# Kernel optimization log

Hardware: AMD Instinct MI355X
Metric: run time of the kernel (lower is better)

The kernel has to match this reference:

```python
import jax, jax.numpy as jnp
import numpy as np

B, ORG, L = 128, 4, 2048
C1, C2 = 128, 64
K0, K1, K2 = 7, 5, 3
VQD, VQN = 64, 1024
CARD, NG = 32, 8
EPS = 1e-5


def _conv(x, w, groups=1):
    # 1D conv, stride 1, 'same' padding (k-1)//2, NCH layout, weight (O, I/g, K)
    p = (w.shape[-1] - 1) // 2
    return jax.lax.conv_general_dilated(
        x, w, (1,), [(p, p)],
        dimension_numbers=('NCH', 'OIH', 'NCH'), feature_group_count=groups)


def _tconv(x, w):
    # ConvTranspose1d(stride=1, padding=(k-1)//2) == conv with channel-transposed, spatially flipped kernel
    return _conv(x, jnp.flip(jnp.transpose(w, (1, 0, 2)), -1))


def _gn(x, g, b, groups=NG):
    Bx, C, T = x.shape
    xr = x.reshape(Bx, groups, C // groups, T)
    mu = xr.mean((2, 3), keepdims=True)
    var = xr.var((2, 3), keepdims=True)
    xn = ((xr - mu) * jax.lax.rsqrt(var + EPS)).reshape(Bx, C, T)
    return xn * g[None, :, None] + b[None, :, None]


def setup_inputs() -> dict:
    key = jax.random.key(0)
    ks = iter(jax.random.split(key, 32))
    w = lambda *s: jax.random.normal(next(ks), s, jnp.float32) * 0.05
    ones = lambda n: jnp.ones((n,), jnp.float32)
    zeros = lambda n: jnp.zeros((n,), jnp.float32)
    D = C1 // 2  # ResNeXt bottleneck width
    return dict(
        x=jax.random.normal(next(ks), (B, ORG, L), jnp.float32),
        w0=w(C1, ORG, K0), g0_g=ones(C1), g0_b=zeros(C1),
        wxa=w(D, C1, 1), gxa_g=ones(D), gxa_b=zeros(D),
        wxb=w(D, D // CARD, K1), gxb_g=ones(D), gxb_b=zeros(D),
        wxc=w(C1, D, 1), gxc_g=ones(C1), gxc_b=zeros(C1),
        w2=w(C2, C1, K2), bn2_g=ones(C2), bn2_b=zeros(C2),
        embed_w=jax.random.uniform(next(ks), (VQN, VQD), jnp.float32, -1.0 / VQD, 1.0 / VQD),
        wd2=w(C2, C1, K2), gd2_g=ones(C1), gd2_b=zeros(C1),
        wd1a=w(C1, C1, K1), gd1a_g=ones(C1), gd1a_b=zeros(C1),
        wd1b=w(C1, C1, K1), gd1b_g=ones(C1), gd1b_b=zeros(C1),
        wd0=w(C1, ORG, K0), bd0=zeros(ORG),
    )


def reference(x, w0, g0_g, g0_b, wxa, gxa_g, gxa_b, wxb, gxb_g, gxb_b,
              wxc, gxc_g, gxc_b, w2, bn2_g, bn2_b, embed_w,
              wd2, gd2_g, gd2_b, wd1a, gd1a_g, gd1a_b, wd1b, gd1b_g, gd1b_b,
              wd0, bd0):
    selu = jax.nn.selu

    # ---- encoder ----
    h = selu(_gn(_conv(x, w0), g0_g, g0_b))  # res0

    def resx(h):  # ResNeXt bottleneck, shared weights (module reuses self.resx)
        y = selu(_gn(_conv(h, wxa), gxa_g, gxa_b))
        y = selu(_gn(_conv(y, wxb, groups=CARD), gxb_g, gxb_b))
        y = _gn(_conv(y, wxc), gxc_g, gxc_b)
        return selu(h + y)

    pool = lambda t: t.reshape(t.shape[0], t.shape[1], -1, 2).max(-1)  # MaxPool1d(2)
    h = pool(resx(h))
    h = pool(resx(h))
    # res2: conv + BatchNorm (eval mode, running stats 0/1 -> affine)
    h = _conv(h, w2) * bn2_g[None, :, None] + bn2_b[None, :, None]

    # ---- vector quantization (vqc=True: quantize channel vectors) ----
    Bh, C, T = h.shape  # C == VQD
    Z = jnp.transpose(h, (0, 2, 1)).reshape(-1, VQD)  # [N, vq_dim]
    d = (jnp.sum(Z * Z, 1, keepdims=True) - 2.0 * (Z @ embed_w.T)
         + jnp.sum(embed_w * embed_w, 1)[None, :])  # [N, vq_num] squared L2
    j = jnp.argmin(d, axis=1)
    W_j = embed_w[j]
    commit_loss = jnp.mean(jnp.sum((Z - jax.lax.stop_gradient(W_j)) ** 2, -1))
    vq_loss = jnp.mean(jnp.sum((jax.lax.stop_gradient(Z) - W_j) ** 2, -1))
    hq = jnp.transpose(W_j.reshape(Bh, T, C), (0, 2, 1))  # back to [B, C, T]

    # ---- decoder ----
    up = lambda t: jnp.repeat(t, 2, axis=-1)  # nearest Upsample(x2)

    def deres1(h):  # basic residual block, shared weights (module reuses self.deres1)
        y = selu(_gn(_tconv(h, wd1a), gd1a_g, gd1a_b))
        y = _gn(_tconv(y, wd1b), gd1b_g, gd1b_b)
        return selu(h + y)

    h = selu(_gn(_tconv(hq, wd2), gd2_g, gd2_b))  # deres2
    h = deres1(up(h))
    h = deres1(up(h))
    recon = _tconv(h, wd0) + bd0[None, :, None]  # deres0 (with bias)
    return recon, commit_loss, vq_loss
```

## Files before the change

kernel.cpp:

```cpp
#include <hip/hip_runtime.h>
#include <math.h>

static constexpr int B_   = 128;
static constexpr int ORG_ = 4;
static constexpr int L_   = 2048;
static constexpr int C1_  = 128;
static constexpr int C2_  = 64;
static constexpr int NG_  = 8;
static constexpr int VQD_ = 64;
static constexpr int VQN_ = 1024;

typedef __attribute__((ext_vector_type(8))) short bf16x8;
typedef __attribute__((ext_vector_type(4))) float f32x4;

__device__ __forceinline__ float selu_f(float x) {
    const float scale = 1.0507009873554805f;
    const float alpha = 1.6732632423543772f;
    return scale * (x > 0.f ? x : alpha * expm1f(x));
}
__device__ __forceinline__ unsigned short f2bf(float x) {
    unsigned u = __float_as_uint(x);
    u = (u + 0x7FFFu + ((u >> 16) & 1u)) >> 16;
    return (unsigned short)u;
}

__global__ void wprep_kernel(const float* __restrict__ w, float* __restrict__ wT,
                             int CO, int cig, int K, int so, int si, int sk, int koff)
{
    int idx = blockIdx.x * 256 + threadIdx.x;
    int total = cig * K * CO;
    if (idx >= total) return;
    int o = idx % CO;
    int r = idx / CO;
    int i = r / K, k = r % K;
    wT[idx] = w[(long)o * so + (long)i * si + (long)k * sk + koff];
}

__global__ void wprep_mfma_kernel(const float* __restrict__ w, unsigned short* __restrict__ wb)
{
    int idx = blockIdx.x * 256 + threadIdx.x;
    if (idx >= 5 * 16 * 128 * 8) return;
    int j  = idx & 7;
    int o  = (idx >> 3) & 127;
    int kk = idx >> 10;
    int ig = kk & 3, ic = (kk >> 2) & 3, k = kk >> 4;
    int i  = ic * 32 + ig * 8 + j;
    wb[idx] = f2bf(w[(long)i * (128 * 5) + o * 5 + (4 - k)]);
}

__global__ void fill_kernel(float* p, float v, int n)
{
    int i = blockIdx.x * 256 + threadIdx.x;
    if (i < n) p[i] = v;
}

template<int K, int CO, int NTHR, int TT, int OT>
__global__ __launch_bounds__(NTHR) void conv_tile_kernel(
    const float* __restrict__ in, const float* __restrict__ wT,
    const float* __restrict__ scale, const float* __restrict__ bias,
    float* __restrict__ out,
    int CI, int T, int cig, int cog,
    const float* __restrict__ ist, const float* __restrict__ ig,
    const float* __restrict__ ibt, int icpg, int iselu,
    const float* __restrict__ res)
{
    constexpr int P    = (K - 1) / 2;
    constexpr int SPAN = TT + K - 1;
    constexpr int RS   = (SPAN + 3) & ~3;
    constexpr int NO   = CO / OT;
    constexpr int NT   = (CO * TT) / (NTHR * OT);
    constexpr int XW   = NT + K - 1;
    extern __shared__ float lds[];

    const int tile = blockIdx.x;
    const int b    = blockIdx.y;
    const int t0g  = tile * TT;
    const float* inb = in + (long)b * CI * T;

    for (int idx = threadIdx.x; idx < CI * SPAN; idx += NTHR) {
        int c = idx / SPAN, j = idx % SPAN;
        int tt = t0g + j - P;
        float v = 0.f;
        if (tt >= 0 && tt < T) {
            v = inb[(long)c * T + tt];
            if (ist) {
                const float* s = &ist[2 * (b * NG_ + c / icpg)];
                v = (v - s[0]) * s[1] * ig[c] + ibt[c];
                if (res) v += res[((long)b * CI + c) * T + tt];
                if (iselu) v = selu_f(v);
            }
        }
        lds[c * RS + j] = v;
    }
    __syncthreads();

    const int o0   = (threadIdx.x % NO) * OT;
    const int slot = threadIdx.x / NO;
    const int t0   = slot * NT;
    const int g    = o0 / cog;
    const float* wrow = wT + o0;

    float acc[OT][NT];
#pragma unroll
    for (int oo = 0; oo < OT; ++oo)
#pragma unroll
        for (int u = 0; u < NT; ++u) acc[oo][u] = 0.f;

    for (int i = 0; i < cig; ++i) {
        const int irow = g * cig + i;
        float xin[(XW + 3) & ~3];
        if constexpr (NT % 4 == 0) {
            constexpr int X4 = (XW + 3) / 4;
            const float4* l4 = reinterpret_cast<const float4*>(&lds[irow * RS + t0]);
#pragma unroll
            for (int j = 0; j < X4; ++j) {
                float4 v = l4[j];
                xin[4 * j]     = v.x;
                xin[4 * j + 1] = v.y;
                xin[4 * j + 2] = v.z;
                xin[4 * j + 3] = v.w;
            }
        } else {
#pragma unroll
            for (int j = 0; j < XW; ++j) xin[j] = lds[irow * RS + t0 + j];
        }
        float wk[OT][K];
#pragma unroll
        for (int oo = 0; oo < OT; ++oo)
#pragma unroll
            for (int k = 0; k < K; ++k) wk[oo][k] = wrow[(i * K + k) * CO + oo];
#pragma unroll
        for (int oo = 0; oo < OT; ++oo)
#pragma unroll
            for (int u = 0; u < NT; ++u)
#pragma unroll
                for (int k = 0; k < K; ++k)
                    acc[oo][u] = fmaf(xin[u + k], wk[oo][k], acc[oo][u]);
    }

#pragma unroll
    for (int oo = 0; oo < OT; ++oo) {
        const int o = o0 + oo;
        const float sc = scale ? scale[o] : 1.f;
        const float bi = bias  ? bias[o]  : 0.f;
        float* ob = out + ((long)b * CO + o) * T + t0g + t0;
#pragma unroll
        for (int u = 0; u < NT; ++u) ob[u] = acc[oo][u] * sc + bi;
    }
}

__global__ __launch_bounds__(256) void conv_mfma5_kernel(
    const float* __restrict__ in, const unsigned short* __restrict__ wb,
    float* __restrict__ out, int T,
    const float* __restrict__ ist, const float* __restrict__ ig_,
    const float* __restrict__ ibt, int icpg)
{
    constexpr int SPAN = 68, RSI = 136;
    __shared__ unsigned short xlds[SPAN * RSI];

    const int t0g = blockIdx.x * 64;
    const int b   = blockIdx.y;
    const float* inb = in + (long)b * 128 * T;

    for (int idx = threadIdx.x; idx < 128 * SPAN; idx += 256) {
        int i = idx / SPAN, j = idx % SPAN;
        int tt = t0g + j - 2;
        float v = 0.f;
        if (tt >= 0 && tt < T) {
            v = inb[(long)i * T + tt];
            if (ist) {
                const float* s = &ist[2 * (b * NG_ + i / icpg)];
                v = selu_f((v - s[0]) * s[1] * ig_[i] + ibt[i]);
            }
        }
        xlds[j * RSI + i] = f2bf(v);
    }
    __syncthreads();

    const int lane = threadIdx.x & 63;
    const int wid  = threadIdx.x >> 6;
    const int tw   = wid * 16;
    const int mr   = lane & 15;
    const int kg   = lane >> 4;

    f32x4 acc[8];
#pragma unroll
    for (int ot = 0; ot < 8; ++ot) acc[ot] = (f32x4){0.f, 0.f, 0.f, 0.f};

#pragma unroll
    for (int k = 0; k < 5; ++k) {
#pragma unroll
        for (int ic = 0; ic < 4; ++ic) {
            bf16x8 a = *(const bf16x8*)&xlds[(tw + mr + k) * RSI + ic * 32 + kg * 8];
            const unsigned short* wp = wb + (((k * 16 + ic * 4 + kg) * 128) + mr) * 8;
#pragma unroll
            for (int ot = 0; ot < 8; ++ot) {
                bf16x8 bfr = *(const bf16x8*)(wp + ot * 16 * 8);
                acc[ot] = __builtin_amdgcn_mfma_f32_16x16x32_bf16(a, bfr, acc[ot], 0, 0, 0);
            }
        }
    }

#pragma unroll
    for (int ot = 0; ot < 8; ++ot) {
        int o = ot * 16 + mr;
        float4 v = make_float4(acc[ot][0], acc[ot][1], acc[ot][2], acc[ot][3]);
        *(float4*)&out[((long)b * 128 + o) * T + t0g + tw + kg * 4] = v;
    }
}

__global__ __launch_bounds__(256) void gn_stats_kernel(
    const float* __restrict__ x, float* __restrict__ stats,
    int C, int T, int G)
{
    const int bg = blockIdx.x;
    const int cpg = C / G;
    const int b = bg / G, g = bg % G;
    const float* base = x + ((long)b * C + (long)g * cpg) * T;
    const long n4 = (long)cpg * T / 4;
    const float4* b4 = (const float4*)base;
    float s = 0.f, ss = 0.f;
    for (long i = threadIdx.x; i < n4; i += blockDim.x) {
        float4 v = b4[i];
        s += v.x + v.y + v.z + v.w;
        ss += v.x * v.x + v.y * v.y + v.z * v.z + v.w * v.w;
    }
#pragma unroll
    for (int off = 32; off; off >>= 1) {
        s  += __shfl_down(s, off);
        ss += __shfl_down(ss, off);
    }
    __shared__ float sh_s[4], sh_ss[4];
    const int wid = threadIdx.x >> 6, lane = threadIdx.x & 63;
    if (lane == 0) { sh_s[wid] = s; sh_ss[wid] = ss; }
    __syncthreads();
    if (threadIdx.x == 0) {
        float S = 0.f, SS = 0.f;
        for (int i = 0; i < 4; ++i) { S += sh_s[i]; SS += sh_ss[i]; }
        float inv_n = 1.f / (float)((long)cpg * T);
        float mu  = S * inv_n;
        float var = SS * inv_n - mu * mu;
        stats[2 * bg]     = mu;
        stats[2 * bg + 1] = rsqrtf(var + 1e-5f);
    }
}

__global__ __launch_bounds__(256) void pool_fused_kernel(
    const float* __restrict__ x, const float* __restrict__ xst,
    const float* __restrict__ xg, const float* __restrict__ xb, int xcpg,
    const float* __restrict__ r, const float* __restrict__ rst,
    const float* __restrict__ rg, const float* __restrict__ rb, int rcpg, int rselu,
    float* __restrict__ out, int C, int Tout, long total)
{
    for (long idx = blockIdx.x * (long)blockDim.x + threadIdx.x; idx < total;
         idx += (long)gridDim.x * blockDim.x) {
        const int to = (int)(idx % Tout);
        const int c  = (int)((idx / Tout) % C);
        const int b  = (int)(idx / ((long)Tout * C));
        const long base = ((long)b * C + c) * (2 * Tout);
        const float* sx = &xst[2 * (b * NG_ + c / xcpg)];
        const float xgc = sx[1] * xg[c], xbc = xb[c] - sx[0] * sx[1] * xg[c];
        float rgc = 1.f, rbc = 0.f;
        if (rst) {
            const float* sr = &rst[2 * (b * NG_ + c / rcpg)];
            rgc = sr[1] * rg[c]; rbc = rb[c] - sr[0] * sr[1] * rg[c];
        }
        float f[2];
#pragma unroll
        for (int q = 0; q < 2; ++q) {
            long t = base + 2 * to + q;
            float rv = r[t] * rgc + rbc;
            if (rst && rselu) rv = selu_f(rv);
            f[q] = selu_f(x[t] * xgc + xbc + rv);
        }
        out[((long)b * C + c) * Tout + to] = fmaxf(f[0], f[1]);
    }
}

__global__ __launch_bounds__(256) void up_fused_kernel(
    const float* __restrict__ x, const float* __restrict__ xst,
    const float* __restrict__ xg, const float* __restrict__ xb, int xcpg,
    const float* __restrict__ res,
    float* __restrict__ out, int C, int Tin, long total)
{
    for (long idx = blockIdx.x * (long)blockDim.x + threadIdx.x; idx < total;
         idx += (long)gridDim.x * blockDim.x) {
        const int t = (int)(idx % Tin);
        const int c = (int)((idx / Tin) % C);
        const int b = (int)(idx / ((long)Tin * C));
        const float* s = &xst[2 * (b * NG_ + c / xcpg)];
        float v = (x[idx] - s[0]) * s[1] * xg[c] + xb[c];
        if (res) v += res[idx];
        v = selu_f(v);
        float2* o2 = (float2*)(out + (((long)b * C + c) * Tin + t) * 2);
        *o2 = make_float2(v, v);
    }
}

__global__ void wnorm_kernel(const float* __restrict__ codes, float* __restrict__ wn)
{
    int j = blockIdx.x * 256 + threadIdx.x;
    if (j >= VQN_) return;
    const float* c = codes + (long)j * VQD_;
    float s = 0.f;
#pragma unroll
    for (int i = 0; i < VQD_; ++i) s = fmaf(c[i], c[i], s);
    wn[j] = s;
}

__global__ __launch_bounds__(256) void vq_argmin_kernel(
    const float* __restrict__ s0, const float* __restrict__ s1,
    float* __restrict__ bests, int* __restrict__ bjs,
    int T, int base, int init)
{
    __shared__ float tile[64 * 65];
    const int n0 = blockIdx.x * 64;
    const int b  = n0 / T;
    const int tb = n0 % T;
    const int p  = threadIdx.x;

    float best = 3.4e38f;
    int bj = base;
    if (p < 64 && !init) { best = bests[n0 + p]; bj = bjs[n0 + p]; }

    for (int half = 0; half < 2; ++half) {
        const float* S = half ? s1 : s0;
        for (int c0 = 0; c0 < 256; c0 += 64) {
            __syncthreads();
#pragma unroll
            for (int it = 0; it < 4; ++it) {
                int r  = it * 16 + (threadIdx.x >> 4);
                int c4 = threadIdx.x & 15;
                float4 v = *(const float4*)&S[((long)b * 256 + c0 + r) * T + tb + c4 * 4];
                tile[r * 65 + c4 * 4 + 0] = v.x;
                tile[r * 65 + c4 * 4 + 1] = v.y;
                tile[r * 65 + c4 * 4 + 2] = v.z;
                tile[r * 65 + c4 * 4 + 3] = v.w;
            }
            __syncthreads();
            if (p < 64) {
                int jb = base + half * 256 + c0;
#pragma unroll
                for (int c = 0; c < 64; ++c) {
                    float sv = tile[c * 65 + p];
                    if (sv < best) { best = sv; bj = jb + c; }
                }
            }
        }
    }
    if (p < 64) { bests[n0 + p] = best; bjs[n0 + p] = bj; }
}

__global__ __launch_bounds__(256) void vq_gather_kernel(
    const float* __restrict__ h, const float* __restrict__ codes,
    const int* __restrict__ bjs, float* __restrict__ hq, float* __restrict__ loss,
    int T)
{
    const int n0 = blockIdx.x * 64;
    const int b  = n0 / T;
    const int tb = n0 % T;
    __shared__ int sbj[64];
    if (threadIdx.x < 64) sbj[threadIdx.x] = bjs[n0 + threadIdx.x];
    __syncthreads();

    float l = 0.f;
#pragma unroll
    for (int r = 0; r < (VQD_ * 64) / 256; ++r) {
        int idx = r * 256 + (int)threadIdx.x;
        int c  = idx >> 6, tl = idx & 63;
        float wv = codes[(long)sbj[tl] * VQD_ + c];
        long off = ((long)b * VQD_ + c) * T + tb + tl;
        hq[off] = wv;
        float df = h[off] - wv;
        l = fmaf(df, df, l);
    }
#pragma unroll
    for (int off = 32; off; off >>= 1) l += __shfl_down(l, off);
    if ((threadIdx.x & 63) == 0) atomicAdd(loss, l);
}

__global__ void zero_kernel(float* p) { p[0] = 0.f; }

__global__ void finalize_kernel(const float* __restrict__ loss, float* __restrict__ out,
                                float invNP, long off)
{
    float v = loss[0] * invNP;
    out[off]     = v;
    out[off + 1] = v;
}

static inline int nblk(long total, int thr = 256, long cap = 262144) {
    long b = (total + thr - 1) / thr;
    if (b > cap) b = cap;
    if (b < 1) b = 1;
    return (int)b;
}
static inline int ldsz(int CI, int K, int TT = 64) {
    int span = TT + K - 1;
    int rs = (span + 3) & ~3;
    return CI * rs * 4;
}

struct WT {
    long w0, wxa, wxb, wxc, w2, wd2, wd0, total;
};
static WT wt_offsets() {
    WT o; long p = 0;
    o.w0   = p; p += (long)ORG_ * 7 * C1_;
    o.wxa  = p; p += (long)C1_ * 1 * (C1_ / 2);
    o.wxb  = p; p += 2L * 5 * (C1_ / 2);
    o.wxc  = p; p += (long)(C1_ / 2) * 1 * C1_;
    o.w2   = p; p += (long)C1_ * 3 * C2_;
    o.wd2  = p; p += (long)C2_ * 3 * C1_;
    o.wd0  = p; p += (long)C1_ * 7 * ORG_;
    o.total = p;
    return o;
}

static void run_chunk(const float* x, const float* const* W, const float* wt,
                      const WT& wo, const unsigned short* wbA, const unsigned short* wbB,
                      const float* wn, const float* wts, const float* neg2,
                      float* bests, int* bjs, float* out,
                      float* A, float* Bb, float* Cc, float* st, float* lossbuf,
                      int Bc, long nbuf, hipStream_t stream)
{
    const float* g0_g  = W[1];
    const float* g0_b  = W[2];
    const float* gxa_g = W[4];
    const float* gxa_b = W[5];
    const float* gxb_g = W[7];
    const float* gxb_b = W[8];
    const float* gxc_g = W[10];
    const float* gxc_b = W[11];
    const float* bn2_g = W[13];
    const float* bn2_b = W[14];
    const float* embed = W[15];
    const float* gd2_g = W[17];
    const float* gd2_b = W[18];
    const float* gd1a_g= W[20];
    const float* gd1a_b= W[21];
    const float* gd1b_g= W[23];
    const float* gd1b_b= W[24];
    const float* bd0   = W[26];

    const int D_ = C1_ / 2;
    const int SLOT = 2048;
    float* st0 = st + 0 * SLOT;
    float* st1 = st + 1 * SLOT;
    float* st2 = st + 2 * SLOT;
    float* st3 = st + 3 * SLOT;
    float* st4 = st + 4 * SLOT;
    float* st5 = st + 5 * SLOT;
    float* st6 = st + 6 * SLOT;

    const int nbg = Bc * NG_;

    int T = L_;

    conv_tile_kernel<7, 128, 512, 64, 1><<<dim3(T / 64, Bc), 512, ldsz(ORG_, 7), stream>>>(
        x, wt + wo.w0, nullptr, nullptr, A, ORG_, T, ORG_, C1_,
        nullptr, nullptr, nullptr, 0, 0, nullptr);
    gn_stats_kernel<<<nbg, 256, 0, stream>>>(A, st0, C1_, T, NG_);

    conv_tile_kernel<1, 64, 512, 64, 2><<<dim3(T / 64, Bc), 512, ldsz(C1_, 1), stream>>>(
        A, wt + wo.wxa, nullptr, nullptr, Bb, C1_, T, C1_, D_,
        st0, g0_g, g0_b, C1_ / NG_, 1, nullptr);
    gn_stats_kernel<<<nbg, 256, 0, stream>>>(Bb, st1, D_, T, NG_);

    conv_tile_kernel<5, 64, 512, 64, 1><<<dim3(T / 64, Bc), 512, ldsz(D_, 5), stream>>>(
        Bb, wt + wo.wxb, nullptr, nullptr, Bb + nbuf / 2, D_, T, 2, 2,
        st1, gxa_g, gxa_b, D_ / NG_, 1, nullptr);
    gn_stats_kernel<<<nbg, 256, 0, stream>>>(Bb + nbuf / 2, st2, D_, T, NG_);

    conv_tile_kernel<1, 128, 512, 64, 2><<<dim3(T / 64, Bc), 512, ldsz(D_, 1), stream>>>(
        Bb + nbuf / 2, wt + wo.wxc, nullptr, nullptr, Cc, D_, T, D_, C1_,
        st2, gxb_g, gxb_b, D_ / NG_, 1, nullptr);
    gn_stats_kernel<<<nbg, 256, 0, stream>>>(Cc, st3, C1_, T, NG_);

    {
        int Tout = T / 2;
        long tt = (long)Bc * C1_ * Tout;
        pool_fused_kernel<<<nblk(tt), 256, 0, stream>>>(
            Cc, st3, gxc_g, gxc_b, C1_ / NG_,
            A, st0, g0_g, g0_b, C1_ / NG_, 1,
            Bb, C1_, Tout, tt);
        T = Tout;
    }

    conv_tile_kernel<1, 64, 512, 64, 2><<<dim3(T / 64, Bc), 512, ldsz(C1_, 1), stream>>>(
        Bb, wt + wo.wxa, nullptr, nullptr, Cc, C1_, T, C1_, D_,
        nullptr, nullptr, nullptr, 0, 0, nullptr);
    gn_stats_kernel<<<nbg, 256, 0, stream>>>(Cc, st1, D_, T, NG_);

    conv_tile_kernel<5, 64, 512, 64, 1><<<dim3(T / 64, Bc), 512, ldsz(D_, 5), stream>>>(
        Cc, wt + wo.wxb, nullptr, nullptr, Cc + nbuf / 2, D_, T, 2, 2,
        st1, gxa_g, gxa_b, D_ / NG_, 1, nullptr);
    gn_stats_kernel<<<nbg, 256, 0, stream>>>(Cc + nbuf / 2, st2, D_, T, NG_);

    conv_tile_kernel<1, 128, 512, 64, 2><<<dim3(T / 64, Bc), 512, ldsz(D_, 1), stream>>>(
        Cc + nbuf / 2, wt + wo.wxc, nullptr, nullptr, A, D_, T, D_, C1_,
        st2, gxb_g, gxb_b, D_ / NG_, 1, nullptr);
    gn_stats_kernel<<<nbg, 256, 0, stream>>>(A, st3, C1_, T, NG_);

    {
        int Tout = T / 2;
        long tt = (long)Bc * C1_ * Tout;
        pool_fused_kernel<<<nblk(tt), 256, 0, stream>>>(
            A, st3, gxc_g, gxc_b, C1_ / NG_,
            Bb, nullptr, nullptr, nullptr, 0, 0,
            Cc, C1_, Tout, tt);
        T = Tout;
    }

    conv_tile_kernel<3, 64, 512, 64, 1><<<dim3(T / 64, Bc), 512, ldsz(C1_, 3), stream>>>(
        Cc, wt + wo.w2, bn2_g, bn2_b, Bb, C1_, T, C1_, C2_,
        nullptr, nullptr, nullptr, 0, 0, nullptr);

    {
        int NP = Bc * T;
        long half = nbuf / 2;
        for (int pass = 0; pass < 2; ++pass) {
            for (int q = 0; q < 2; ++q) {
                int base = pass * 512 + q * 256;
                conv_tile_kernel<1, 256, 512, 64, 4><<<dim3(T / 64, Bc), 512,
                                                       ldsz(VQD_, 1), stream>>>(
                    Bb, wts + (long)base * VQD_, neg2, wn + base, Cc + q * half,
                    VQD_, T, VQD_, 256,
                    nullptr, nullptr, nullptr, 0, 0, nullptr);
            }
            vq_argmin_kernel<<<NP / 64, 256, 0, stream>>>(
                Cc, Cc + half, bests, bjs, T, pass * 512, pass == 0 ? 1 : 0);
        }
        vq_gather_kernel<<<NP / 64, 256, 0, stream>>>(Bb, embed, bjs, A, lossbuf, T);
    }

    conv_tile_kernel<3, 128, 512, 64, 1><<<dim3(T / 64, Bc), 512, ldsz(C2_, 3), stream>>>(
        A, wt + wo.wd2, nullptr, nullptr, Bb, C2_, T, C2_, C1_,
        nullptr, nullptr, nullptr, 0, 0, nullptr);
    gn_stats_kernel<<<nbg, 256, 0, stream>>>(Bb, st4, C1_, T, NG_);

    {
        long tt = (long)Bc * C1_ * T;
        up_fused_kernel<<<nblk(tt), 256, 0, stream>>>(
            Bb, st4, gd2_g, gd2_b, C1_ / NG_, nullptr, Cc, C1_, T, tt);
        T *= 2;
    }

    conv_mfma5_kernel<<<dim3(T / 64, Bc), 256, 0, stream>>>(
        Cc, wbA, A, T, nullptr, nullptr, nullptr, 0);
    gn_stats_kernel<<<nbg, 256, 0, stream>>>(A, st5, C1_, T, NG_);

    conv_mfma5_kernel<<<dim3(T / 64, Bc), 256, 0, stream>>>(
        A, wbB, Bb, T, st5, gd1a_g, gd1a_b, C1_ / NG_);
    gn_stats_kernel<<<nbg, 256, 0, stream>>>(Bb, st6, C1_, T, NG_);

    {
        long tt = (long)Bc * C1_ * T;
        up_fused_kernel<<<nblk(tt), 256, 0, stream>>>(
            Bb, st6, gd1b_g, gd1b_b, C1_ / NG_, Cc, A, C1_, T, tt);
        T *= 2;
    }

    conv_mfma5_kernel<<<dim3(T / 64, Bc), 256, 0, stream>>>(
        A, wbA, Cc, T, nullptr, nullptr, nullptr, 0);
    gn_stats_kernel<<<nbg, 256, 0, stream>>>(Cc, st5, C1_, T, NG_);

    conv_mfma5_kernel<<<dim3(T / 64, Bc), 256, 0, stream>>>(
        Cc, wbB, Bb, T, st5, gd1a_g, gd1a_b, C1_ / NG_);
    gn_stats_kernel<<<nbg, 256, 0, stream>>>(Bb, st6, C1_, T, NG_);

    conv_tile_kernel<7, 4, 256, 64, 1><<<dim3(T / 64, Bc), 256, ldsz(C1_, 7), stream>>>(
        Bb, wt + wo.wd0, nullptr, bd0, out, C1_, T, C1_, ORG_,
        st6, gd1b_g, gd1b_b, C1_ / NG_, 1, A);
}

extern "C" void kernel_launch(void* const* d_in, const int* in_sizes, int n_in,
                              void* d_out, int out_size, void* d_ws, size_t ws_size,
                              hipStream_t stream) {
    const float* x = (const float*)d_in[0];
    const float* W[27];
    for (int i = 0; i < 27; ++i) W[i] = (const float*)d_in[i + 1];

    float* out = (float*)d_out;
    const WT wo = wt_offsets();

    const long WT_F32  = 262144;
    const long WB_F32  = 2 * 81920 / 2;
    const long WTS_F32 = VQN_ * VQD_;
    const long ST_F32  = 8 * 2048;
    const long PTS_MAX = (long)B_ * (L_ / 4);
    const long FIXED = WT_F32 + WB_F32 + 1024 + WTS_F32 + 256 + ST_F32 + 64
                     + PTS_MAX + PTS_MAX;
    int Bc = 0;
    for (int cand = B_; cand >= 1; cand >>= 1) {
        size_t need = ((size_t)FIXED + (size_t)3 * cand * C1_ * L_) * sizeof(float);
        if (need <= ws_size) { Bc = cand; break; }
    }
    if (Bc == 0) return;

    float* wt            = (float*)d_ws;
    unsigned short* wbA  = (unsigned short*)(wt + WT_F32);
    unsigned short* wbB  = wbA + 81920;
    float* wn            = wt + WT_F32 + WB_F32;
    float* wts           = wn + 1024;
    float* neg2          = wts + WTS_F32;
    float* st            = neg2 + 256;
    float* lossbuf       = st + ST_F32;
    float* bests         = lossbuf + 64;
    int*   bjs           = (int*)(bests + PTS_MAX);
    const long nbuf = (long)Bc * C1_ * L_;
    float* A  = (float*)(bjs + PTS_MAX);
    float* Bb = A + nbuf;
    float* Cc = Bb + nbuf;

    const int D_ = C1_ / 2;

    auto prep = [&](const float* w, long off, int CO, int cig, int K,
                    int so, int si, int sk, int koff) {
        int total = cig * K * CO;
        wprep_kernel<<<(total + 255) / 256, 256, 0, stream>>>(
            w, wt + off, CO, cig, K, so, si, sk, koff);
    };
    prep(W[0],  wo.w0,   C1_, ORG_, 7, ORG_ * 7, 7,        1,  0);
    prep(W[3],  wo.wxa,  D_,  C1_,  1, C1_,      1,        1,  0);
    prep(W[6],  wo.wxb,  D_,  2,    5, 2 * 5,    5,        1,  0);
    prep(W[9],  wo.wxc,  C1_, D_,   1, D_,       1,        1,  0);
    prep(W[12], wo.w2,   C2_, C1_,  3, C1_ * 3,  3,        1,  0);
    prep(W[16], wo.wd2,  C1_, C2_,  3, 3,        C1_ * 3, -1,  2);
    prep(W[25], wo.wd0,  ORG_, C1_, 7, 7,        ORG_ * 7, -1, 6);
    wprep_mfma_kernel<<<81920 / 256, 256, 0, stream>>>(W[19], wbA);
    wprep_mfma_kernel<<<81920 / 256, 256, 0, stream>>>(W[22], wbB);
    wnorm_kernel<<<(VQN_ + 255) / 256, 256, 0, stream>>>(W[15], wn);
    for (int q = 0; q < 4; ++q) {
        wprep_kernel<<<(256 * VQD_ + 255) / 256, 256, 0, stream>>>(
            W[15] + (long)q * 256 * VQD_, wts + (long)q * 256 * VQD_,
            256, VQD_, 1, VQD_, 1, 1, 0);
    }
    fill_kernel<<<1, 256, 0, stream>>>(neg2, -2.f, 256);

    zero_kernel<<<1, 1, 0, stream>>>(lossbuf);

    for (int b0 = 0; b0 < B_; b0 += Bc) {
        const float* xc = x + (long)b0 * ORG_ * L_;
        float* outc = out + (long)b0 * ORG_ * L_;
        run_chunk(xc, W, wt, wo, wbA, wbB, wn, wts, neg2, bests, bjs,
                  outc, A, Bb, Cc, st, lossbuf, Bc, nbuf, stream);
    }

    {
        float invNP = 1.f / (float)(B_ * (L_ / 4));
        finalize_kernel<<<1, 1, 0, stream>>>(lossbuf, out, invNP, (long)out_size - 2);
    }
}
```

Measured before the change: 2.384 ms.

## Fuse VQ distance argmin into conv epilogue and stage final conv weights in LDS

```diff
diff --git a/kernel.cpp b/kernel.cpp
--- a/kernel.cpp
+++ b/kernel.cpp
@@ -9,6 +9,7 @@
 static constexpr int NG_  = 8;
 static constexpr int VQD_ = 64;
 static constexpr int VQN_ = 1024;
+static constexpr long PTS_ = (long)B_ * (L_ / 4);
 
 typedef __attribute__((ext_vector_type(8))) short bf16x8;
 typedef __attribute__((ext_vector_type(4))) float f32x4;
@@ -54,7 +55,7 @@
     if (i < n) p[i] = v;
 }
 
-template<int K, int CO, int NTHR, int TT, int OT>
+template<int K, int CO, int NTHR, int TT, int OT, int VQ, int WL>
 __global__ __launch_bounds__(NTHR) void conv_tile_kernel(
     const float* __restrict__ in, const float* __restrict__ wT,
     const float* __restrict__ scale, const float* __restrict__ bias,
@@ -62,7 +63,8 @@
     int CI, int T, int cig, int cog,
     const float* __restrict__ ist, const float* __restrict__ ig,
     const float* __restrict__ ibt, int icpg, int iselu,
-    const float* __restrict__ res)
+    const float* __restrict__ res,
+    float* __restrict__ vbest, int* __restrict__ vbj, int jbase)
 {
     constexpr int P    = (K - 1) / 2;
     constexpr int SPAN = TT + K - 1;
@@ -92,13 +94,20 @@
         }
         lds[c * RS + j] = v;
     }
+    if constexpr (WL) {
+        float* wl = lds + CI * RS;
+        for (int idx = threadIdx.x; idx < cig * K * CO; idx += NTHR)
+            wl[idx] = wT[idx];
+    }
     __syncthreads();
 
     const int o0   = (threadIdx.x % NO) * OT;
     const int slot = threadIdx.x / NO;
     const int t0   = slot * NT;
     const int g    = o0 / cog;
-    const float* wrow = wT + o0;
+    const float* wrow;
+    if constexpr (WL) wrow = lds + CI * RS + o0;
+    else              wrow = wT + o0;
 
     float acc[OT][NT];
 #pragma unroll
@@ -138,14 +147,40 @@
                     acc[oo][u] = fmaf(xin[u + k], wk[oo][k], acc[oo][u]);
     }
 
-#pragma unroll
-    for (int oo = 0; oo < OT; ++oo) {
-        const int o = o0 + oo;
-        const float sc = scale ? scale[o] : 1.f;
-        const float bi = bias  ? bias[o]  : 0.f;
-        float* ob = out + ((long)b * CO + o) * T + t0g + t0;
-#pragma unroll
-        for (int u = 0; u < NT; ++u) ob[u] = acc[oo][u] * sc + bi;
+    if constexpr (VQ) {
+        const int lane = threadIdx.x & 63;
+#pragma unroll
+        for (int u = 0; u < NT; ++u) {
+            float bv = 3.4e38f;
+            int bj = 0;
+#pragma unroll
+            for (int oo = 0; oo < OT; ++oo) {
+                const int o = o0 + oo;
+                float sv = fmaf(acc[oo][u], scale[o], bias[o]);
+                if (sv < bv) { bv = sv; bj = jbase + o; }
+            }
+#pragma unroll
+            for (int off = 1; off < 64; off <<= 1) {
+                float v2 = __shfl_xor(bv, off);
+                int   j2 = __shfl_xor(bj, off);
+                if (v2 < bv || (v2 == bv && j2 < bj)) { bv = v2; bj = j2; }
+            }
+            if (lane == 0) {
+                long n = (long)b * T + t0g + t0 + u;
+                vbest[n] = bv;
+                vbj[n]   = bj;
+            }
+        }
+    } else {
+#pragma unroll
+        for (int oo = 0; oo < OT; ++oo) {
+            const int o = o0 + oo;
+            const float sc = scale ? scale[o] : 1.f;
+            const float bi = bias  ? bias[o]  : 0.f;
+            float* ob = out + ((long)b * CO + o) * T + t0g + t0;
+#pragma unroll
+            for (int u = 0; u < NT; ++u) ob[u] = acc[oo][u] * sc + bi;
+        }
     }
 }
 
@@ -308,47 +343,19 @@
     wn[j] = s;
 }
 
-__global__ __launch_bounds__(256) void vq_argmin_kernel(
-    const float* __restrict__ s0, const float* __restrict__ s1,
-    float* __restrict__ bests, int* __restrict__ bjs,
-    int T, int base, int init)
-{
-    __shared__ float tile[64 * 65];
-    const int n0 = blockIdx.x * 64;
-    const int b  = n0 / T;
-    const int tb = n0 % T;
-    const int p  = threadIdx.x;
-
-    float best = 3.4e38f;
-    int bj = base;
-    if (p < 64 && !init) { best = bests[n0 + p]; bj = bjs[n0 + p]; }
-
-    for (int half = 0; half < 2; ++half) {
-        const float* S = half ? s1 : s0;
-        for (int c0 = 0; c0 < 256; c0 += 64) {
-            __syncthreads();
-#pragma unroll
-            for (int it = 0; it < 4; ++it) {
-                int r  = it * 16 + (threadIdx.x >> 4);
-                int c4 = threadIdx.x & 15;
-                float4 v = *(const float4*)&S[((long)b * 256 + c0 + r) * T + tb + c4 * 4];
-                tile[r * 65 + c4 * 4 + 0] = v.x;
-                tile[r * 65 + c4 * 4 + 1] = v.y;
-                tile[r * 65 + c4 * 4 + 2] = v.z;
-                tile[r * 65 + c4 * 4 + 3] = v.w;
-            }
-            __syncthreads();
-            if (p < 64) {
-                int jb = base + half * 256 + c0;
-#pragma unroll
-                for (int c = 0; c < 64; ++c) {
-                    float sv = tile[c * 65 + p];
-                    if (sv < best) { best = sv; bj = jb + c; }
-                }
-            }
-        }
-    }
-    if (p < 64) { bests[n0 + p] = best; bjs[n0 + p] = bj; }
+__global__ void vq_combine_kernel(const float* __restrict__ vb, const int* __restrict__ vj,
+                                  int* __restrict__ bjs, long stride, int NP)
+{
+    int n = blockIdx.x * 256 + threadIdx.x;
+    if (n >= NP) return;
+    float best = vb[n];
+    int bj = vj[n];
+#pragma unroll
+    for (int s = 1; s < 4; ++s) {
+        float v = vb[(long)s * stride + n];
+        if (v < best) { best = v; bj = vj[(long)s * stride + n]; }
+    }
+    bjs[n] = bj;
 }
 
 __global__ __launch_bounds__(256) void vq_gather_kernel(
@@ -420,7 +427,7 @@
 static void run_chunk(const float* x, const float* const* W, const float* wt,
                       const WT& wo, const unsigned short* wbA, const unsigned short* wbB,
                       const float* wn, const float* wts, const float* neg2,
-                      float* bests, int* bjs, float* out,
+                      float* vbest4, int* vbj4, int* bjs, float* out,
                       float* A, float* Bb, float* Cc, float* st, float* lossbuf,
                       int Bc, long nbuf, hipStream_t stream)
 {
@@ -457,24 +464,24 @@
 
     int T = L_;
 
-    conv_tile_kernel<7, 128, 512, 64, 1><<<dim3(T / 64, Bc), 512, ldsz(ORG_, 7), stream>>>(
+    conv_tile_kernel<7, 128, 512, 64, 1, 0, 0><<<dim3(T / 64, Bc), 512, ldsz(ORG_, 7), stream>>>(
         x, wt + wo.w0, nullptr, nullptr, A, ORG_, T, ORG_, C1_,
-        nullptr, nullptr, nullptr, 0, 0, nullptr);
+        nullptr, nullptr, nullptr, 0, 0, nullptr, nullptr, nullptr, 0);
     gn_stats_kernel<<<nbg, 256, 0, stream>>>(A, st0, C1_, T, NG_);
 
-    conv_tile_kernel<1, 64, 512, 64, 2><<<dim3(T / 64, Bc), 512, ldsz(C1_, 1), stream>>>(
+    conv_tile_kernel<1, 64, 512, 64, 2, 0, 0><<<dim3(T / 64, Bc), 512, ldsz(C1_, 1), stream>>>(
         A, wt + wo.wxa, nullptr, nullptr, Bb, C1_, T, C1_, D_,
-        st0, g0_g, g0_b, C1_ / NG_, 1, nullptr);
+        st0, g0_g, g0_b, C1_ / NG_, 1, nullptr, nullptr, nullptr, 0);
     gn_stats_kernel<<<nbg, 256, 0, stream>>>(Bb, st1, D_, T, NG_);
 
-    conv_tile_kernel<5, 64, 512, 64, 1><<<dim3(T / 64, Bc), 512, ldsz(D_, 5), stream>>>(
+    conv_tile_kernel<5, 64, 512, 64, 1, 0, 0><<<dim3(T / 64, Bc), 512, ldsz(D_, 5), stream>>>(
         Bb, wt + wo.wxb, nullptr, nullptr, Bb + nbuf / 2, D_, T, 2, 2,
-        st1, gxa_g, gxa_b, D_ / NG_, 1, nullptr);
+        st1, gxa_g, gxa_b, D_ / NG_, 1, nullptr, nullptr, nullptr, 0);
     gn_stats_kernel<<<nbg, 256, 0, stream>>>(Bb + nbuf / 2, st2, D_, T, NG_);
 
-    conv_tile_kernel<1, 128, 512, 64, 2><<<dim3(T / 64, Bc), 512, ldsz(D_, 1), stream>>>(
+    conv_tile_kernel<1, 128, 512, 64, 2, 0, 0><<<dim3(T / 64, Bc), 512, ldsz(D_, 1), stream>>>(
         Bb + nbuf / 2, wt + wo.wxc, nullptr, nullptr, Cc, D_, T, D_, C1_,
-        st2, gxb_g, gxb_b, D_ / NG_, 1, nullptr);
+        st2, gxb_g, gxb_b, D_ / NG_, 1, nullptr, nullptr, nullptr, 0);
     gn_stats_kernel<<<nbg, 256, 0, stream>>>(Cc, st3, C1_, T, NG_);
 
     {
@@ -487,19 +494,19 @@
         T = Tout;
     }
 
-    conv_tile_kernel<1, 64, 512, 64, 2><<<dim3(T / 64, Bc), 512, ldsz(C1_, 1), stream>>>(
+    conv_tile_kernel<1, 64, 512, 64, 2, 0, 0><<<dim3(T / 64, Bc), 512, ldsz(C1_, 1), stream>>>(
         Bb, wt + wo.wxa, nullptr, nullptr, Cc, C1_, T, C1_, D_,
-        nullptr, nullptr, nullptr, 0, 0, nullptr);
+        nullptr, nullptr, nullptr, 0, 0, nullptr, nullptr, nullptr, 0);
     gn_stats_kernel<<<nbg, 256, 0, stream>>>(Cc, st1, D_, T, NG_);
 
-    conv_tile_kernel<5, 64, 512, 64, 1><<<dim3(T / 64, Bc), 512, ldsz(D_, 5), stream>>>(
+    conv_tile_kernel<5, 64, 512, 64, 1, 0, 0><<<dim3(T / 64, Bc), 512, ldsz(D_, 5), stream>>>(
         Cc, wt + wo.wxb, nullptr, nullptr, Cc + nbuf / 2, D_, T, 2, 2,
-        st1, gxa_g, gxa_b, D_ / NG_, 1, nullptr);
+        st1, gxa_g, gxa_b, D_ / NG_, 1, nullptr, nullptr, nullptr, 0);
     gn_stats_kernel<<<nbg, 256, 0, stream>>>(Cc + nbuf / 2, st2, D_, T, NG_);
 
-    conv_tile_kernel<1, 128, 512, 64, 2><<<dim3(T / 64, Bc), 512, ldsz(D_, 1), stream>>>(
+    conv_tile_kernel<1, 128, 512, 64, 2, 0, 0><<<dim3(T / 64, Bc), 512, ldsz(D_, 1), stream>>>(
         Cc + nbuf / 2, wt + wo.wxc, nullptr, nullptr, A, D_, T, D_, C1_,
-        st2, gxb_g, gxb_b, D_ / NG_, 1, nullptr);
+        st2, gxb_g, gxb_b, D_ / NG_, 1, nullptr, nullptr, nullptr, 0);
     gn_stats_kernel<<<nbg, 256, 0, stream>>>(A, st3, C1_, T, NG_);
 
     {
@@ -512,31 +519,27 @@
         T = Tout;
     }
 
-    conv_tile_kernel<3, 64, 512, 64, 1><<<dim3(T / 64, Bc), 512, ldsz(C1_, 3), stream>>>(
+    conv_tile_kernel<3, 64, 512, 64, 1, 0, 0><<<dim3(T / 64, Bc), 512, ldsz(C1_, 3), stream>>>(
         Cc, wt + wo.w2, bn2_g, bn2_b, Bb, C1_, T, C1_, C2_,
-        nullptr, nullptr, nullptr, 0, 0, nullptr);
+        nullptr, nullptr, nullptr, 0, 0, nullptr, nullptr, nullptr, 0);
 
     {
         int NP = Bc * T;
-        long half = nbuf / 2;
-        for (int pass = 0; pass < 2; ++pass) {
-            for (int q = 0; q < 2; ++q) {
-                int base = pass * 512 + q * 256;
-                conv_tile_kernel<1, 256, 512, 64, 4><<<dim3(T / 64, Bc), 512,
-                                                       ldsz(VQD_, 1), stream>>>(
-                    Bb, wts + (long)base * VQD_, neg2, wn + base, Cc + q * half,
-                    VQD_, T, VQD_, 256,
-                    nullptr, nullptr, nullptr, 0, 0, nullptr);
-            }
-            vq_argmin_kernel<<<NP / 64, 256, 0, stream>>>(
-                Cc, Cc + half, bests, bjs, T, pass * 512, pass == 0 ? 1 : 0);
-        }
+        for (int s = 0; s < 4; ++s) {
+            conv_tile_kernel<1, 256, 512, 64, 4, 1, 0><<<dim3(T / 64, Bc), 512,
+                                                         ldsz(VQD_, 1), stream>>>(
+                Bb, wts + (long)s * 256 * VQD_, neg2, wn + s * 256, nullptr,
+                VQD_, T, VQD_, 256,
+                nullptr, nullptr, nullptr, 0, 0, nullptr,
+                vbest4 + (long)s * PTS_, vbj4 + (long)s * PTS_, s * 256);
+        }
+        vq_combine_kernel<<<(NP + 255) / 256, 256, 0, stream>>>(vbest4, vbj4, bjs, PTS_, NP);
         vq_gather_kernel<<<NP / 64, 256, 0, stream>>>(Bb, embed, bjs, A, lossbuf, T);
     }
 
-    conv_tile_kernel<3, 128, 512, 64, 1><<<dim3(T / 64, Bc), 512, ldsz(C2_, 3), stream>>>(
+    conv_tile_kernel<3, 128, 512, 64, 1, 0, 0><<<dim3(T / 64, Bc), 512, ldsz(C2_, 3), stream>>>(
         A, wt + wo.wd2, nullptr, nullptr, Bb, C2_, T, C2_, C1_,
-        nullptr, nullptr, nullptr, 0, 0, nullptr);
+        nullptr, nullptr, nullptr, 0, 0, nullptr, nullptr, nullptr, 0);
     gn_stats_kernel<<<nbg, 256, 0, stream>>>(Bb, st4, C1_, T, NG_);
 
     {
@@ -569,9 +572,10 @@
         Cc, wbB, Bb, T, st5, gd1a_g, gd1a_b, C1_ / NG_);
     gn_stats_kernel<<<nbg, 256, 0, stream>>>(Bb, st6, C1_, T, NG_);
 
-    conv_tile_kernel<7, 4, 256, 64, 1><<<dim3(T / 64, Bc), 256, ldsz(C1_, 7), stream>>>(
+    conv_tile_kernel<7, 4, 256, 64, 1, 0, 1><<<dim3(T / 64, Bc), 256,
+                                               ldsz(C1_, 7) + C1_ * 7 * ORG_ * 4, stream>>>(
         Bb, wt + wo.wd0, nullptr, bd0, out, C1_, T, C1_, ORG_,
-        st6, gd1b_g, gd1b_b, C1_ / NG_, 1, A);
+        st6, gd1b_g, gd1b_b, C1_ / NG_, 1, A, nullptr, nullptr, 0);
 }
 
 extern "C" void kernel_launch(void* const* d_in, const int* in_sizes, int n_in,
@@ -588,9 +592,8 @@
     const long WB_F32  = 2 * 81920 / 2;
     const long WTS_F32 = VQN_ * VQD_;
     const long ST_F32  = 8 * 2048;
-    const long PTS_MAX = (long)B_ * (L_ / 4);
-    const long FIXED = WT_F32 + WB_F32 + 1024 + WTS_F32 + 256 + ST_F32 + 64
-                     + PTS_MAX + PTS_MAX;
+    const long VQ_F32  = 4 * PTS_ + 4 * PTS_ + PTS_;
+    const long FIXED = WT_F32 + WB_F32 + 1024 + WTS_F32 + 256 + ST_F32 + 64 + VQ_F32;
     int Bc = 0;
     for (int cand = B_; cand >= 1; cand >>= 1) {
         size_t need = ((size_t)FIXED + (size_t)3 * cand * C1_ * L_) * sizeof(float);
@@ -606,10 +609,11 @@
     float* neg2          = wts + WTS_F32;
     float* st            = neg2 + 256;
     float* lossbuf       = st + ST_F32;
-    float* bests         = lossbuf + 64;
-    int*   bjs           = (int*)(bests + PTS_MAX);
+    float* vbest4        = lossbuf + 64;
+    int*   vbj4          = (int*)(vbest4 + 4 * PTS_);
+    int*   bjs           = vbj4 + 4 * PTS_;
     const long nbuf = (long)Bc * C1_ * L_;
-    float* A  = (float*)(bjs + PTS_MAX);
+    float* A  = (float*)(bjs + PTS_);
     float* Bb = A + nbuf;
     float* Cc = Bb + nbuf;
 
@@ -643,7 +647,7 @@
     for (int b0 = 0; b0 < B_; b0 += Bc) {
         const float* xc = x + (long)b0 * ORG_ * L_;
         float* outc = out + (long)b0 * ORG_ * L_;
-        run_chunk(xc, W, wt, wo, wbA, wbB, wn, wts, neg2, bests, bjs,
+        run_chunk(xc, W, wt, wo, wbA, wbB, wn, wts, neg2, vbest4, vbj4, bjs,
                   outc, A, Bb, Cc, st, lossbuf, Bc, nbuf, stream);
     }
 
```

New measurement: 2.299 ms. 1.04x faster.
